# Kernel tuning notes

Measured on AMD Instinct MI355X. Metric: run time of the kernel, lower is better.

The kernel has to match this reference:

```python
import jax, jax.numpy as jnp
import numpy as np

N_HEAD = 8
WINDOW = 22   # sliding window size from get_mask()
TRAIN = 29    # per-segment length cap from get_mask()


def _build_mask(T):
    # Banded (sliding-window causal) mask on one segment, tiled 3x3 over segments.
    t = T // 3
    m = np.triu(np.ones((TRAIN, TRAIN), dtype=bool), 1)
    for i in range(WINDOW, TRAIN):
        m[i, : i - WINDOW + 1] = True
    m = np.tile(m[:t, :t], (3, 3))  # [T, T], True = masked out
    return jnp.asarray(m)


def setup_inputs() -> dict:
    key = jax.random.key(0)
    ks = jax.random.split(key, 5)
    B, T, C = 512, 87, 512
    s = 0.02
    return {
        "x": jax.random.normal(ks[0], (B, T, C), dtype=jnp.float32),
        "Wq": jax.random.normal(ks[1], (C, C), dtype=jnp.float32) * s,
        "bq": jnp.zeros((C,), dtype=jnp.float32),
        "Wk": jax.random.normal(ks[2], (C, C), dtype=jnp.float32) * s,
        "bk": jnp.zeros((C,), dtype=jnp.float32),
        "Wv": jax.random.normal(ks[3], (C, C), dtype=jnp.float32) * s,
        "bv": jnp.zeros((C,), dtype=jnp.float32),
        "Wp": jax.random.normal(ks[4], (C, C), dtype=jnp.float32) * s,
        "bp": jnp.zeros((C,), dtype=jnp.float32),
    }


def reference(x, Wq, bq, Wk, bk, Wv, bv, Wp, bp):
    B, T, C = x.shape
    H = N_HEAD
    D = C // H
    # nn.Linear: y = x @ W.T + b
    def split_heads(y):
        return y.reshape(B, T, H, D).transpose(0, 2, 1, 3)  # [B,H,T,D]
    q = split_heads(x @ Wq.T + bq)
    k = split_heads(x @ Wk.T + bk)
    v = split_heads(x @ Wv.T + bv)
    att = jnp.einsum("bhqd,bhkd->bhqk", q, k) * (1.0 / jnp.sqrt(jnp.float32(D)))
    mask = _build_mask(T)  # [T,T] True = disallowed
    att = jnp.where(mask[None, None], -jnp.inf, att)
    att = jax.nn.softmax(att, axis=-1)
    # dropout layers are identity in eval mode
    y = jnp.einsum("bhqk,bhkd->bhqd", att, v)
    y = y.transpose(0, 2, 1, 3).reshape(B, T, C)
    return y @ Wp.T + bp
```

## Files before the change

kernel.cpp:

```cpp
#include <hip/hip_runtime.h>
#include <hip/hip_bf16.h>
#include <stdint.h>

#define B_   512
#define T_   87
#define C_   512
#define H_   8
#define D_   64
#define BT_  44544
#define BH_  4096

typedef __attribute__((ext_vector_type(4))) float f32x4;
typedef __attribute__((ext_vector_type(8))) __bf16 bf16x8;
typedef __attribute__((ext_vector_type(4))) unsigned short u16x4;

__device__ __forceinline__ int mod29(int x) {
  return x < 29 ? x : (x < 58 ? x - 29 : x - 58);
}


__global__ void convert_x_kernel(const float* __restrict__ x,
                                 __hip_bfloat16* __restrict__ xb, int n4) {
  int stride = gridDim.x * blockDim.x;
  for (int i = blockIdx.x * blockDim.x + threadIdx.x; i < n4; i += stride) {
    f32x4 v = ((const f32x4*)x)[i];
    u16x4 o;
    o.x = __builtin_bit_cast(unsigned short, __float2bfloat16(v.x));
    o.y = __builtin_bit_cast(unsigned short, __float2bfloat16(v.y));
    o.z = __builtin_bit_cast(unsigned short, __float2bfloat16(v.z));
    o.w = __builtin_bit_cast(unsigned short, __float2bfloat16(v.w));
    ((u16x4*)xb)[i] = o;
  }
}

__global__ void convert_w_kernel(const float* __restrict__ Wq, const float* __restrict__ Wk,
                                 const float* __restrict__ Wv, const float* __restrict__ Wp,
                                 const float* __restrict__ bq, const float* __restrict__ bk,
                                 const float* __restrict__ bv,
                                 __hip_bfloat16* __restrict__ wqkv,
                                 __hip_bfloat16* __restrict__ wp,
                                 float* __restrict__ biasc) {
  const int NW = 262144;
  const int total = 3 * NW + NW + 1536;
  int stride = gridDim.x * blockDim.x;
  for (int i = blockIdx.x * blockDim.x + threadIdx.x; i < total; i += stride) {
    if (i < 3 * NW) {
      float v = (i < NW) ? Wq[i] : (i < 2 * NW ? Wk[i - NW] : Wv[i - 2 * NW]);
      wqkv[i] = __float2bfloat16(v);
    } else if (i < 4 * NW) {
      wp[i - 3 * NW] = __float2bfloat16(Wp[i - 3 * NW]);
    } else {
      int j = i - 4 * NW;
      biasc[j] = (j < 512) ? bq[j] : (j < 1024 ? bk[j - 512] : bv[j - 1024]);
    }
  }
}


template<int FM, int FN>
__device__ __forceinline__ void compute_tile(const char* Ab, const char* Bb,
                                             int wbM, int wbN, int r16, int r4,
                                             f32x4 acc[FM][FN]) {
  const int cxor = (r16 & 7) << 4;
  bf16x8 bf[FN][2];
#pragma unroll
  for (int fn = 0; fn < FN; ++fn) {
    int row = wbN + fn * 16 + r16;
#pragma unroll
    for (int kk = 0; kk < 2; ++kk)
      bf[fn][kk] = *(const bf16x8*)(Bb + row * 128 + ((kk * 64 + r4 * 16) ^ cxor));
  }
#pragma unroll
  for (int fm = 0; fm < FM; ++fm) {
    int row = wbM + fm * 16 + r16;
    bf16x8 a0 = *(const bf16x8*)(Ab + row * 128 + ((r4 * 16) ^ cxor));
    bf16x8 a1 = *(const bf16x8*)(Ab + row * 128 + ((64 + r4 * 16) ^ cxor));
#pragma unroll
    for (int fn = 0; fn < FN; ++fn) {
      acc[fm][fn] = __builtin_amdgcn_mfma_f32_16x16x32_bf16(a0, bf[fn][0], acc[fm][fn], 0, 0, 0);
      acc[fm][fn] = __builtin_amdgcn_mfma_f32_16x16x32_bf16(a1, bf[fn][1], acc[fm][fn], 0, 0, 0);
    }
  }
}

template<int EPI>
__global__ __launch_bounds__(256) void gemmr_kernel(
    const __hip_bfloat16* __restrict__ A, const __hip_bfloat16* __restrict__ Bt,
    const float* __restrict__ bias, int ntn,
    void* __restrict__ o0, void* __restrict__ o1, void* __restrict__ o2) {
  __shared__ __align__(16) char smem[2][2][16384];

  int tid = threadIdx.x, lane = tid & 63, wave = tid >> 6;
  int r16 = lane & 15, r4 = lane >> 4;

  int nwg = gridDim.x;
  int wg = (blockIdx.x & 7) * (nwg >> 3) + (blockIdx.x >> 3);
  int tileM = (wg / ntn) * 128, tileN = (wg % ntn) * 128;

  int wr = wave >> 1, wc = wave & 1;
  int wbM = wr * 64, wbN = wc * 64;

  const int rbase = tid >> 3, c = tid & 7;
  const int cs = (c ^ (rbase & 7)) << 4;
  const char* Ag = (const char*)A + (size_t)(tileM + rbase) * 1024 + c * 16;
  const char* Bg = (const char*)Bt + (size_t)(tileN + rbase) * 1024 + c * 16;

  f32x4 acc[4][4] = {};
  bf16x8 rA[4], rB[4];

#pragma unroll
  for (int j = 0; j < 4; ++j) {
    rA[j] = *(const bf16x8*)(Ag + (size_t)j * 32768);
    rB[j] = *(const bf16x8*)(Bg + (size_t)j * 32768);
  }
#pragma unroll
  for (int j = 0; j < 4; ++j) {
    *(bf16x8*)(&smem[0][0][0] + (rbase + 32 * j) * 128 + cs) = rA[j];
    *(bf16x8*)(&smem[0][1][0] + (rbase + 32 * j) * 128 + cs) = rB[j];
  }
  __syncthreads();

#pragma unroll
  for (int kt = 0; kt < 8; ++kt) {
    int cur = kt & 1;
    if (kt < 7) {
#pragma unroll
      for (int j = 0; j < 4; ++j) {
        rA[j] = *(const bf16x8*)(Ag + (size_t)j * 32768 + (kt + 1) * 128);
        rB[j] = *(const bf16x8*)(Bg + (size_t)j * 32768 + (kt + 1) * 128);
      }
    }
    __builtin_amdgcn_s_setprio(1);
    compute_tile<4, 4>(&smem[cur][0][0], &smem[cur][1][0], wbM, wbN, r16, r4, acc);
    __builtin_amdgcn_s_setprio(0);
    if (kt < 7) {
#pragma unroll
      for (int j = 0; j < 4; ++j) {
        *(bf16x8*)(&smem[cur ^ 1][0][0] + (rbase + 32 * j) * 128 + cs) = rA[j];
        *(bf16x8*)(&smem[cur ^ 1][1][0] + (rbase + 32 * j) * 128 + cs) = rB[j];
      }
    }
    __syncthreads();
  }

  if constexpr (EPI == 0) {
    char* scratch = &smem[0][0][0] + wave * 2304;
    int gn0 = tileN + wbN;
    int sel = gn0 >> 9;
    int hh = (gn0 & 511) >> 6;
    __hip_bfloat16* obase = (sel == 0) ? (__hip_bfloat16*)o0
                          : (sel == 1) ? (__hip_bfloat16*)o1 : (__hip_bfloat16*)o2;
#pragma unroll
    for (int fm = 0; fm < 4; ++fm) {
#pragma unroll
      for (int fn = 0; fn < 4; ++fn) {
        float bv = bias[gn0 + fn * 16 + r16];
#pragma unroll
        for (int rr = 0; rr < 4; ++rr)
          *(__hip_bfloat16*)(scratch + (r4 * 4 + rr) * 144 + (fn * 16 + r16) * 2) =
              __float2bfloat16(acc[fm][fn][rr] + bv);
      }
#pragma unroll
      for (int p = 0; p < 2; ++p) {
        bf16x8 vrow = *(const bf16x8*)(scratch + (p * 8 + (lane >> 3)) * 144 + (lane & 7) * 16);
        int gm = tileM + wbM + fm * 16 + p * 8 + (lane >> 3);
        int bb = gm / 87, tt = gm - bb * 87;
        *(bf16x8*)(obase + ((size_t)(bb * 8 + hh) * 96 + tt) * 64 + (lane & 7) * 8) = vrow;
      }
    }
  } else {
    char* scratch = &smem[0][0][0] + wave * 4352;
#pragma unroll
    for (int fm = 0; fm < 4; ++fm) {
#pragma unroll
      for (int fn = 0; fn < 4; ++fn) {
        float bv = bias[tileN + wbN + fn * 16 + r16];
#pragma unroll
        for (int rr = 0; rr < 4; ++rr)
          *(float*)(scratch + (r4 * 4 + rr) * 272 + (fn * 16 + r16) * 4) =
              acc[fm][fn][rr] + bv;
      }
#pragma unroll
      for (int p = 0; p < 4; ++p) {
        f32x4 vr = *(const f32x4*)(scratch + (p * 4 + (lane >> 4)) * 272 + (lane & 15) * 16);
        int gm = tileM + wbM + fm * 16 + p * 4 + (lane >> 4);
        *(f32x4*)((float*)o0 + (size_t)gm * 512 + tileN + wbN + (lane & 15) * 4) = vr;
      }
    }
  }
}

#define QS_O  0
#define KS_O  13824
#define VT_O  27648
#define PB_O  40960

__global__ __launch_bounds__(256) void attn_kernel(
    const __hip_bfloat16* __restrict__ q_ws, const __hip_bfloat16* __restrict__ k_ws,
    const __hip_bfloat16* __restrict__ v_ws, __hip_bfloat16* __restrict__ y_ws) {
  __shared__ __align__(16) char smem[60928];

  int tid = threadIdx.x, lane = tid & 63, wave = tid >> 6;
  int bh = blockIdx.x, b = bh >> 3, h = bh & 7;
  int r16 = lane & 15, r4 = lane >> 4;

  {
    const bf16x8* gq = (const bf16x8*)(q_ws + (size_t)bh * 6144);
    const bf16x8* gk = (const bf16x8*)(k_ws + (size_t)bh * 6144);
    const bf16x8* gv = (const bf16x8*)(v_ws + (size_t)bh * 6144);
    for (int i = tid; i < 768; i += 256) {
      int row = i >> 3, ch = i & 7;
      *(bf16x8*)(smem + QS_O + row * 144 + ch * 16) = gq[i];
      *(bf16x8*)(smem + KS_O + row * 144 + ch * 16) = gk[i];
      bf16x8 v8 = gv[i];
      int tc = row >> 3, tb = (row & 7) << 1, xr = ch & 3;
#pragma unroll
      for (int e = 0; e < 8; ++e) {
        int d = ch * 8 + e;
        *(__bf16*)(smem + VT_O + d * 208 + ((tc ^ xr) << 4) + tb) = v8[e];
      }
    }
  }
  __syncthreads();

  int ljv[6]; bool cok[6];
#pragma unroll
  for (int j = 0; j < 6; ++j) {
    int col = j * 16 + r16;
    ljv[j] = mod29(col);
    cok[j] = col < 87;
  }

  for (int m = wave; m < 6; m += 4) {
    f32x4 s[6] = {};
#pragma unroll
    for (int kk = 0; kk < 2; ++kk) {
      bf16x8 aq = *(const bf16x8*)(smem + QS_O + (m * 16 + r16) * 144 + kk * 64 + r4 * 16);
#pragma unroll
      for (int j = 0; j < 6; ++j) {
        bf16x8 kb = *(const bf16x8*)(smem + KS_O + (j * 16 + r16) * 144 + kk * 64 + r4 * 16);
        s[j] = __builtin_amdgcn_mfma_f32_16x16x32_bf16(aq, kb, s[j], 0, 0, 0);
      }
    }
#pragma unroll
    for (int rr = 0; rr < 4; ++rr) {
      int row = m * 16 + r4 * 4 + rr;
      bool rok = row < 87;
      int lr = mod29(row);
      float mxv = -1e30f;
#pragma unroll
      for (int j = 0; j < 6; ++j) {
        bool al = rok && cok[j] && (ljv[j] <= lr) && (ljv[j] + 21 >= lr);
        float sv = al ? s[j][rr] * 0.125f : -1e30f;
        s[j][rr] = sv;
        mxv = fmaxf(mxv, sv);
      }
      mxv = fmaxf(mxv, __shfl_xor(mxv, 1));
      mxv = fmaxf(mxv, __shfl_xor(mxv, 2));
      mxv = fmaxf(mxv, __shfl_xor(mxv, 4));
      mxv = fmaxf(mxv, __shfl_xor(mxv, 8));
      float sm = 0.f;
#pragma unroll
      for (int j = 0; j < 6; ++j) {
        float e = __expf(s[j][rr] - mxv);
        s[j][rr] = e;
        sm += e;
      }
      sm += __shfl_xor(sm, 1);
      sm += __shfl_xor(sm, 2);
      sm += __shfl_xor(sm, 4);
      sm += __shfl_xor(sm, 8);
      float inv = rok ? 1.f / sm : 0.f;
#pragma unroll
      for (int j = 0; j < 6; ++j)
        *(__hip_bfloat16*)(smem + PB_O + row * 208 + (j * 16 + r16) * 2) =
            __float2bfloat16(s[j][rr] * inv);
    }
  }
  __syncthreads();

  for (int p = 0; p < 6; ++p) {
    int pair = wave + p * 4;
    int mt = pair >> 2, nt = pair & 3;
    int d = nt * 16 + r16;
    int dx = (d >> 3) & 3;
    f32x4 acc = {0.f, 0.f, 0.f, 0.f};
#pragma unroll
    for (int kk = 0; kk < 3; ++kk) {
      bf16x8 a  = *(const bf16x8*)(smem + PB_O + (mt * 16 + r16) * 208 + kk * 64 + r4 * 16);
      bf16x8 bb = *(const bf16x8*)(smem + VT_O + d * 208 + (((kk * 4 + r4) ^ dx) << 4));
      acc = __builtin_amdgcn_mfma_f32_16x16x32_bf16(a, bb, acc, 0, 0, 0);
    }
    int t0 = mt * 16 + r4 * 4;
#pragma unroll
    for (int r = 0; r < 4; ++r) {
      int t = t0 + r;
      if (t < 87)
        y_ws[((size_t)b * 87 + t) * 512 + h * 64 + d] = __float2bfloat16(acc[r]);
    }
  }
}

extern "C" void kernel_launch(void* const* d_in, const int* in_sizes, int n_in,
                              void* d_out, int out_size, void* d_ws, size_t ws_size,
                              hipStream_t stream) {
  const float* x  = (const float*)d_in[0];
  const float* Wq = (const float*)d_in[1];
  const float* bq = (const float*)d_in[2];
  const float* Wk = (const float*)d_in[3];
  const float* bk = (const float*)d_in[4];
  const float* Wv = (const float*)d_in[5];
  const float* bv = (const float*)d_in[6];
  const float* Wp = (const float*)d_in[7];
  const float* bp = (const float*)d_in[8];
  float* out = (float*)d_out;

  char* ws = (char*)d_ws;
  size_t off = 0;
  __hip_bfloat16* xb    = (__hip_bfloat16*)(ws + off); off += (size_t)BT_ * 512 * 2;
  __hip_bfloat16* wqkv  = (__hip_bfloat16*)(ws + off); off += 1536 * 512 * 2;
  __hip_bfloat16* wp    = (__hip_bfloat16*)(ws + off); off += 512 * 512 * 2;
  float*          biasc = (float*)(ws + off);          off += 8192;
  __hip_bfloat16* q_ws  = (__hip_bfloat16*)(ws + off); off += (size_t)BH_ * 6144 * 2;
  __hip_bfloat16* k_ws  = (__hip_bfloat16*)(ws + off); off += (size_t)BH_ * 6144 * 2;
  __hip_bfloat16* v_ws  = (__hip_bfloat16*)(ws + off); off += (size_t)BH_ * 6144 * 2;
  __hip_bfloat16* yb = xb;

  if (ws_size < off) return;

  convert_x_kernel<<<2048, 256, 0, stream>>>(x, xb, BT_ * 512 / 4);
  convert_w_kernel<<<1024, 256, 0, stream>>>(Wq, Wk, Wv, Wp, bq, bk, bv, wqkv, wp, biasc);
  gemmr_kernel<0><<<4176, 256, 0, stream>>>(xb, wqkv, biasc, 12, q_ws, k_ws, v_ws);
  attn_kernel<<<BH_, 256, 0, stream>>>(q_ws, k_ws, v_ws, yb);
  gemmr_kernel<1><<<1392, 256, 0, stream>>>(yb, wp, bp, 4, out, nullptr, nullptr);
}
```

Measured before the change: 237.7 us.

## Fuse x fp32-to-bf16 conversion into QKV GEMM and coalesce attention output stores

Removes the separate convert_x kernel. The QKV GEMM now reads fp32 x directly and converts it to bf16 while staging into shared memory, which saves a full write and re-read of the bf16 copy of x. The catch is that each of the 12 N-tiles re-reads the fp32 A rows, so A-side global traffic per tile doubles. Separately, the attention kernel now stages its output through LDS and writes 16-byte rows, replacing scattered 2-byte stores.

```diff
diff --git a/kernel.cpp b/kernel.cpp
--- a/kernel.cpp
+++ b/kernel.cpp
@@ -13,24 +13,23 @@
 typedef __attribute__((ext_vector_type(4))) float f32x4;
 typedef __attribute__((ext_vector_type(8))) __bf16 bf16x8;
 typedef __attribute__((ext_vector_type(4))) unsigned short u16x4;
+typedef __attribute__((ext_vector_type(8))) unsigned short u16x8;
 
 __device__ __forceinline__ int mod29(int x) {
   return x < 29 ? x : (x < 58 ? x - 29 : x - 58);
 }
 
-
-__global__ void convert_x_kernel(const float* __restrict__ x,
-                                 __hip_bfloat16* __restrict__ xb, int n4) {
-  int stride = gridDim.x * blockDim.x;
-  for (int i = blockIdx.x * blockDim.x + threadIdx.x; i < n4; i += stride) {
-    f32x4 v = ((const f32x4*)x)[i];
-    u16x4 o;
-    o.x = __builtin_bit_cast(unsigned short, __float2bfloat16(v.x));
-    o.y = __builtin_bit_cast(unsigned short, __float2bfloat16(v.y));
-    o.z = __builtin_bit_cast(unsigned short, __float2bfloat16(v.z));
-    o.w = __builtin_bit_cast(unsigned short, __float2bfloat16(v.w));
-    ((u16x4*)xb)[i] = o;
-  }
+__device__ __forceinline__ bf16x8 cvt8(f32x4 a, f32x4 b) {
+  u16x8 u;
+  u[0] = __builtin_bit_cast(unsigned short, __float2bfloat16(a.x));
+  u[1] = __builtin_bit_cast(unsigned short, __float2bfloat16(a.y));
+  u[2] = __builtin_bit_cast(unsigned short, __float2bfloat16(a.z));
+  u[3] = __builtin_bit_cast(unsigned short, __float2bfloat16(a.w));
+  u[4] = __builtin_bit_cast(unsigned short, __float2bfloat16(b.x));
+  u[5] = __builtin_bit_cast(unsigned short, __float2bfloat16(b.y));
+  u[6] = __builtin_bit_cast(unsigned short, __float2bfloat16(b.z));
+  u[7] = __builtin_bit_cast(unsigned short, __float2bfloat16(b.w));
+  return __builtin_bit_cast(bf16x8, u);
 }
 
 __global__ void convert_w_kernel(const float* __restrict__ Wq, const float* __restrict__ Wk,
@@ -56,7 +55,6 @@
   }
 }
 
-
 template<int FM, int FN>
 __device__ __forceinline__ void compute_tile(const char* Ab, const char* Bb,
                                              int wbM, int wbN, int r16, int r4,
@@ -83,10 +81,9 @@
   }
 }
 
-template<int EPI>
-__global__ __launch_bounds__(256) void gemmr_kernel(
-    const __hip_bfloat16* __restrict__ A, const __hip_bfloat16* __restrict__ Bt,
-    const float* __restrict__ bias, int ntn,
+__global__ __launch_bounds__(256) void gemmq_kernel(
+    const float* __restrict__ A, const __hip_bfloat16* __restrict__ Bt,
+    const float* __restrict__ bias,
     void* __restrict__ o0, void* __restrict__ o1, void* __restrict__ o2) {
   __shared__ __align__(16) char smem[2][2][16384];
 
@@ -95,27 +92,29 @@
 
   int nwg = gridDim.x;
   int wg = (blockIdx.x & 7) * (nwg >> 3) + (blockIdx.x >> 3);
-  int tileM = (wg / ntn) * 128, tileN = (wg % ntn) * 128;
+  int tileM = (wg / 12) * 128, tileN = (wg % 12) * 128;
 
   int wr = wave >> 1, wc = wave & 1;
   int wbM = wr * 64, wbN = wc * 64;
 
   const int rbase = tid >> 3, c = tid & 7;
   const int cs = (c ^ (rbase & 7)) << 4;
-  const char* Ag = (const char*)A + (size_t)(tileM + rbase) * 1024 + c * 16;
+  const char* Ag = (const char*)A + (size_t)(tileM + rbase) * 2048 + c * 32;
   const char* Bg = (const char*)Bt + (size_t)(tileN + rbase) * 1024 + c * 16;
 
   f32x4 acc[4][4] = {};
-  bf16x8 rA[4], rB[4];
+  f32x4 rAf[8];
+  bf16x8 rB[4];
 
 #pragma unroll
   for (int j = 0; j < 4; ++j) {
-    rA[j] = *(const bf16x8*)(Ag + (size_t)j * 32768);
+    rAf[2 * j]     = *(const f32x4*)(Ag + (size_t)j * 65536);
+    rAf[2 * j + 1] = *(const f32x4*)(Ag + (size_t)j * 65536 + 16);
     rB[j] = *(const bf16x8*)(Bg + (size_t)j * 32768);
   }
 #pragma unroll
   for (int j = 0; j < 4; ++j) {
-    *(bf16x8*)(&smem[0][0][0] + (rbase + 32 * j) * 128 + cs) = rA[j];
+    *(bf16x8*)(&smem[0][0][0] + (rbase + 32 * j) * 128 + cs) = cvt8(rAf[2 * j], rAf[2 * j + 1]);
     *(bf16x8*)(&smem[0][1][0] + (rbase + 32 * j) * 128 + cs) = rB[j];
   }
   __syncthreads();
@@ -126,7 +125,8 @@
     if (kt < 7) {
 #pragma unroll
       for (int j = 0; j < 4; ++j) {
-        rA[j] = *(const bf16x8*)(Ag + (size_t)j * 32768 + (kt + 1) * 128);
+        rAf[2 * j]     = *(const f32x4*)(Ag + (size_t)j * 65536 + (kt + 1) * 256);
+        rAf[2 * j + 1] = *(const f32x4*)(Ag + (size_t)j * 65536 + (kt + 1) * 256 + 16);
         rB[j] = *(const bf16x8*)(Bg + (size_t)j * 32768 + (kt + 1) * 128);
       }
     }
@@ -136,14 +136,14 @@
     if (kt < 7) {
 #pragma unroll
       for (int j = 0; j < 4; ++j) {
-        *(bf16x8*)(&smem[cur ^ 1][0][0] + (rbase + 32 * j) * 128 + cs) = rA[j];
+        *(bf16x8*)(&smem[cur ^ 1][0][0] + (rbase + 32 * j) * 128 + cs) = cvt8(rAf[2 * j], rAf[2 * j + 1]);
         *(bf16x8*)(&smem[cur ^ 1][1][0] + (rbase + 32 * j) * 128 + cs) = rB[j];
       }
     }
     __syncthreads();
   }
 
-  if constexpr (EPI == 0) {
+  {
     char* scratch = &smem[0][0][0] + wave * 2304;
     int gn0 = tileN + wbN;
     int sel = gn0 >> 9;
@@ -168,7 +168,68 @@
         *(bf16x8*)(obase + ((size_t)(bb * 8 + hh) * 96 + tt) * 64 + (lane & 7) * 8) = vrow;
       }
     }
-  } else {
+  }
+}
+
+__global__ __launch_bounds__(256) void gemmr_kernel(
+    const __hip_bfloat16* __restrict__ A, const __hip_bfloat16* __restrict__ Bt,
+    const float* __restrict__ bias, int ntn, float* __restrict__ out) {
+  __shared__ __align__(16) char smem[2][2][16384];
+
+  int tid = threadIdx.x, lane = tid & 63, wave = tid >> 6;
+  int r16 = lane & 15, r4 = lane >> 4;
+
+  int nwg = gridDim.x;
+  int wg = (blockIdx.x & 7) * (nwg >> 3) + (blockIdx.x >> 3);
+  int tileM = (wg / ntn) * 128, tileN = (wg % ntn) * 128;
+
+  int wr = wave >> 1, wc = wave & 1;
+  int wbM = wr * 64, wbN = wc * 64;
+
+  const int rbase = tid >> 3, c = tid & 7;
+  const int cs = (c ^ (rbase & 7)) << 4;
+  const char* Ag = (const char*)A + (size_t)(tileM + rbase) * 1024 + c * 16;
+  const char* Bg = (const char*)Bt + (size_t)(tileN + rbase) * 1024 + c * 16;
+
+  f32x4 acc[4][4] = {};
+  bf16x8 rA[4], rB[4];
+
+#pragma unroll
+  for (int j = 0; j < 4; ++j) {
+    rA[j] = *(const bf16x8*)(Ag + (size_t)j * 32768);
+    rB[j] = *(const bf16x8*)(Bg + (size_t)j * 32768);
+  }
+#pragma unroll
+  for (int j = 0; j < 4; ++j) {
+    *(bf16x8*)(&smem[0][0][0] + (rbase + 32 * j) * 128 + cs) = rA[j];
+    *(bf16x8*)(&smem[0][1][0] + (rbase + 32 * j) * 128 + cs) = rB[j];
+  }
+  __syncthreads();
+
+#pragma unroll
+  for (int kt = 0; kt < 8; ++kt) {
+    int cur = kt & 1;
+    if (kt < 7) {
+#pragma unroll
+      for (int j = 0; j < 4; ++j) {
+        rA[j] = *(const bf16x8*)(Ag + (size_t)j * 32768 + (kt + 1) * 128);
+        rB[j] = *(const bf16x8*)(Bg + (size_t)j * 32768 + (kt + 1) * 128);
+      }
+    }
+    __builtin_amdgcn_s_setprio(1);
+    compute_tile<4, 4>(&smem[cur][0][0], &smem[cur][1][0], wbM, wbN, r16, r4, acc);
+    __builtin_amdgcn_s_setprio(0);
+    if (kt < 7) {
+#pragma unroll
+      for (int j = 0; j < 4; ++j) {
+        *(bf16x8*)(&smem[cur ^ 1][0][0] + (rbase + 32 * j) * 128 + cs) = rA[j];
+        *(bf16x8*)(&smem[cur ^ 1][1][0] + (rbase + 32 * j) * 128 + cs) = rB[j];
+      }
+    }
+    __syncthreads();
+  }
+
+  {
     char* scratch = &smem[0][0][0] + wave * 4352;
 #pragma unroll
     for (int fm = 0; fm < 4; ++fm) {
@@ -184,7 +245,7 @@
       for (int p = 0; p < 4; ++p) {
         f32x4 vr = *(const f32x4*)(scratch + (p * 4 + (lane >> 4)) * 272 + (lane & 15) * 16);
         int gm = tileM + wbM + fm * 16 + p * 4 + (lane >> 4);
-        *(f32x4*)((float*)o0 + (size_t)gm * 512 + tileN + wbN + (lane & 15) * 4) = vr;
+        *(f32x4*)(out + (size_t)gm * 512 + tileN + wbN + (lane & 15) * 4) = vr;
       }
     }
   }
@@ -293,10 +354,17 @@
     }
     int t0 = mt * 16 + r4 * 4;
 #pragma unroll
-    for (int r = 0; r < 4; ++r) {
-      int t = t0 + r;
-      if (t < 87)
-        y_ws[((size_t)b * 87 + t) * 512 + h * 64 + d] = __float2bfloat16(acc[r]);
+    for (int r = 0; r < 4; ++r)
+      *(__bf16*)(smem + QS_O + (t0 + r) * 136 + d * 2) =
+          __builtin_bit_cast(__bf16, (unsigned short)__builtin_bit_cast(unsigned short, __float2bfloat16(acc[r])));
+  }
+  __syncthreads();
+
+  for (int i = tid; i < 768; i += 256) {
+    int row = i >> 3, ch = i & 7;
+    if (row < 87) {
+      bf16x8 vrow = *(const bf16x8*)(smem + QS_O + row * 136 + ch * 16);
+      *(bf16x8*)((char*)y_ws + ((size_t)b * 87 + row) * 1024 + h * 128 + ch * 16) = vrow;
     }
   }
 }
@@ -317,20 +385,18 @@
 
   char* ws = (char*)d_ws;
   size_t off = 0;
-  __hip_bfloat16* xb    = (__hip_bfloat16*)(ws + off); off += (size_t)BT_ * 512 * 2;
+  __hip_bfloat16* yb    = (__hip_bfloat16*)(ws + off); off += (size_t)BT_ * 512 * 2;
   __hip_bfloat16* wqkv  = (__hip_bfloat16*)(ws + off); off += 1536 * 512 * 2;
   __hip_bfloat16* wp    = (__hip_bfloat16*)(ws + off); off += 512 * 512 * 2;
   float*          biasc = (float*)(ws + off);          off += 8192;
   __hip_bfloat16* q_ws  = (__hip_bfloat16*)(ws + off); off += (size_t)BH_ * 6144 * 2;
   __hip_bfloat16* k_ws  = (__hip_bfloat16*)(ws + off); off += (size_t)BH_ * 6144 * 2;
   __hip_bfloat16* v_ws  = (__hip_bfloat16*)(ws + off); off += (size_t)BH_ * 6144 * 2;
-  __hip_bfloat16* yb = xb;
 
   if (ws_size < off) return;
 
-  convert_x_kernel<<<2048, 256, 0, stream>>>(x, xb, BT_ * 512 / 4);
   convert_w_kernel<<<1024, 256, 0, stream>>>(Wq, Wk, Wv, Wp, bq, bk, bv, wqkv, wp, biasc);
-  gemmr_kernel<0><<<4176, 256, 0, stream>>>(xb, wqkv, biasc, 12, q_ws, k_ws, v_ws);
+  gemmq_kernel<<<4176, 256, 0, stream>>>(x, wqkv, biasc, q_ws, k_ws, v_ws);
   attn_kernel<<<BH_, 256, 0, stream>>>(q_ws, k_ws, v_ws, yb);
-  gemmr_kernel<1><<<1392, 256, 0, stream>>>(yb, wp, bp, 4, out, nullptr, nullptr);
-}
+  gemmr_kernel<<<1392, 256, 0, stream>>>(yb, wp, bp, 4, out);
+}
```

New measurement: 269.2 us. +13.3%, slower.

## Rewrite GEMMs as 256x256 8-wave tiles with direct global-to-LDS 4-stage pipeline

Applied to the files above, without the earlier changes.

Replaces the 128x128 4-wave GEMM with a 256x256, 512-thread kernel that stages A/B panels straight into LDS using global_load_lds, ring-buffered over four slots with explicit vmcnt waits and barriers that interleave loads with MFMA phases. The goal is more reuse per LDS byte, no register round-trip for staging, and overlap of memory with compute. The XCD-aware block remap now handles grids that are not a multiple of 8. Separately, the attention epilogue stages its output through LDS so it can write coalesced 16-byte rows instead of scattered scalar bf16 stores. The trade-offs are fewer workgroups (1044 and 348), which may lower occupancy and hurt tail balance, and heavier LDS use.

```diff
diff --git a/kernel.cpp b/kernel.cpp
--- a/kernel.cpp
+++ b/kernel.cpp
@@ -13,6 +13,17 @@
 typedef __attribute__((ext_vector_type(4))) float f32x4;
 typedef __attribute__((ext_vector_type(8))) __bf16 bf16x8;
 typedef __attribute__((ext_vector_type(4))) unsigned short u16x4;
+
+__device__ __forceinline__ void gl_lds16(const void* g, void* l) {
+  __builtin_amdgcn_global_load_lds(
+      (const __attribute__((address_space(1))) unsigned int*)g,
+      (__attribute__((address_space(3))) unsigned int*)l, 16, 0, 0);
+}
+
+template<int N>
+__device__ __forceinline__ void waitv() {
+  asm volatile("s_waitcnt vmcnt(%0)" :: "i"(N) : "memory");
+}
 
 __device__ __forceinline__ int mod29(int x) {
   return x < 29 ? x : (x < 58 ? x - 29 : x - 58);
@@ -57,101 +68,126 @@
 }
 
 
-template<int FM, int FN>
-__device__ __forceinline__ void compute_tile(const char* Ab, const char* Bb,
-                                             int wbM, int wbN, int r16, int r4,
-                                             f32x4 acc[FM][FN]) {
-  const int cxor = (r16 & 7) << 4;
-  bf16x8 bf[FN][2];
-#pragma unroll
-  for (int fn = 0; fn < FN; ++fn) {
-    int row = wbN + fn * 16 + r16;
-#pragma unroll
-    for (int kk = 0; kk < 2; ++kk)
-      bf[fn][kk] = *(const bf16x8*)(Bb + row * 128 + ((kk * 64 + r4 * 16) ^ cxor));
-  }
-#pragma unroll
-  for (int fm = 0; fm < FM; ++fm) {
-    int row = wbM + fm * 16 + r16;
-    bf16x8 a0 = *(const bf16x8*)(Ab + row * 128 + ((r4 * 16) ^ cxor));
-    bf16x8 a1 = *(const bf16x8*)(Ab + row * 128 + ((64 + r4 * 16) ^ cxor));
-#pragma unroll
-    for (int fn = 0; fn < FN; ++fn) {
-      acc[fm][fn] = __builtin_amdgcn_mfma_f32_16x16x32_bf16(a0, bf[fn][0], acc[fm][fn], 0, 0, 0);
-      acc[fm][fn] = __builtin_amdgcn_mfma_f32_16x16x32_bf16(a1, bf[fn][1], acc[fm][fn], 0, 0, 0);
-    }
-  }
-}
+__device__ __forceinline__ void stage_panel(const char* g, int kbyte, char* dst,
+                                            int wave, int lane) {
+  int rl = lane >> 2, s = lane & 3;
+#pragma unroll
+  for (int j = 0; j < 2; ++j) {
+    int rbase = j * 128 + wave * 16;
+    int row = rbase + rl;
+    int colsw = ((s ^ ((row >> 1) & 3)) << 4);
+    gl_lds16(g + (size_t)row * 1024 + kbyte + colsw, dst + rbase * 64);
+  }
+}
+
+#define PHASE_SEP() __builtin_amdgcn_sched_barrier(0)
 
 template<int EPI>
-__global__ __launch_bounds__(256) void gemmr_kernel(
+__global__ __launch_bounds__(512, 2) void gemm8_kernel(
     const __hip_bfloat16* __restrict__ A, const __hip_bfloat16* __restrict__ Bt,
     const float* __restrict__ bias, int ntn,
     void* __restrict__ o0, void* __restrict__ o1, void* __restrict__ o2) {
-  __shared__ __align__(16) char smem[2][2][16384];
+  constexpr int SLOT = 32768;
+  constexpr int BOFF = 16384;
+  __shared__ __align__(16) char smem[4 * SLOT];
 
   int tid = threadIdx.x, lane = tid & 63, wave = tid >> 6;
   int r16 = lane & 15, r4 = lane >> 4;
 
   int nwg = gridDim.x;
-  int wg = (blockIdx.x & 7) * (nwg >> 3) + (blockIdx.x >> 3);
-  int tileM = (wg / ntn) * 128, tileN = (wg % ntn) * 128;
-
-  int wr = wave >> 1, wc = wave & 1;
-  int wbM = wr * 64, wbN = wc * 64;
-
-  const int rbase = tid >> 3, c = tid & 7;
-  const int cs = (c ^ (rbase & 7)) << 4;
-  const char* Ag = (const char*)A + (size_t)(tileM + rbase) * 1024 + c * 16;
-  const char* Bg = (const char*)Bt + (size_t)(tileN + rbase) * 1024 + c * 16;
-
-  f32x4 acc[4][4] = {};
-  bf16x8 rA[4], rB[4];
-
-#pragma unroll
-  for (int j = 0; j < 4; ++j) {
-    rA[j] = *(const bf16x8*)(Ag + (size_t)j * 32768);
-    rB[j] = *(const bf16x8*)(Bg + (size_t)j * 32768);
-  }
-#pragma unroll
-  for (int j = 0; j < 4; ++j) {
-    *(bf16x8*)(&smem[0][0][0] + (rbase + 32 * j) * 128 + cs) = rA[j];
-    *(bf16x8*)(&smem[0][1][0] + (rbase + 32 * j) * 128 + cs) = rB[j];
-  }
-  __syncthreads();
-
-#pragma unroll
-  for (int kt = 0; kt < 8; ++kt) {
-    int cur = kt & 1;
-    if (kt < 7) {
-#pragma unroll
-      for (int j = 0; j < 4; ++j) {
-        rA[j] = *(const bf16x8*)(Ag + (size_t)j * 32768 + (kt + 1) * 128);
-        rB[j] = *(const bf16x8*)(Bg + (size_t)j * 32768 + (kt + 1) * 128);
-      }
-    }
+  int xcd = blockIdx.x & 7, idx = blockIdx.x >> 3;
+  int q8 = nwg >> 3, r8 = nwg & 7;
+  int wg = (xcd < r8 ? xcd * (q8 + 1) : r8 * (q8 + 1) + (xcd - r8) * q8) + idx;
+  int tileM = (wg / ntn) * 256, tileN = (wg % ntn) * 256;
+
+  int wr = wave >> 2, wc = wave & 3;
+  int wbM = wr * 128, wbN = wc * 64;
+
+  f32x4 acc[8][4] = {};
+
+  const char* Ag = (const char*)A + (size_t)tileM * 1024;
+  const char* Bg = (const char*)Bt + (size_t)tileN * 1024;
+
+  int arow[8], brow[4];
+#pragma unroll
+  for (int fm = 0; fm < 8; ++fm) arow[fm] = wbM + fm * 16 + r16;
+#pragma unroll
+  for (int fn = 0; fn < 4; ++fn) brow[fn] = wbN + fn * 16 + r16;
+
+  stage_panel(Ag, 0, smem, wave, lane);
+  stage_panel(Bg, 0, smem + BOFF, wave, lane);
+  stage_panel(Ag, 64, smem + SLOT, wave, lane);
+  stage_panel(Bg, 64, smem + SLOT + BOFF, wave, lane);
+
+#pragma unroll
+  for (int kt = 0; kt < 16; ++kt) {
+    if (kt < 15) waitv<4>(); else waitv<0>();
+    PHASE_SEP();
+    __builtin_amdgcn_s_barrier();
+    PHASE_SEP();
+
+    const char* cb = smem + (kt & 3) * SLOT;
+    char* nb = smem + ((kt + 2) & 3) * SLOT;
+    bool st = kt < 14;
+
+    bf16x8 bfr[4], afr[4];
+#pragma unroll
+    for (int fn = 0; fn < 4; ++fn)
+      bfr[fn] = *(const bf16x8*)(cb + BOFF + brow[fn] * 64 +
+                                 ((r4 ^ ((brow[fn] >> 1) & 3)) << 4));
+#pragma unroll
+    for (int fm = 0; fm < 4; ++fm)
+      afr[fm] = *(const bf16x8*)(cb + arow[fm] * 64 +
+                                 ((r4 ^ ((arow[fm] >> 1) & 3)) << 4));
+    if (st) stage_panel(Ag, (kt + 2) * 64, nb, wave, lane);
+    PHASE_SEP();
+    __builtin_amdgcn_s_barrier();
+    asm volatile("s_waitcnt lgkmcnt(0)" ::: "memory");
+    PHASE_SEP();
     __builtin_amdgcn_s_setprio(1);
-    compute_tile<4, 4>(&smem[cur][0][0], &smem[cur][1][0], wbM, wbN, r16, r4, acc);
+#pragma unroll
+    for (int fm = 0; fm < 4; ++fm)
+#pragma unroll
+      for (int fn = 0; fn < 4; ++fn)
+        acc[fm][fn] = __builtin_amdgcn_mfma_f32_16x16x32_bf16(afr[fm], bfr[fn],
+                                                              acc[fm][fn], 0, 0, 0);
     __builtin_amdgcn_s_setprio(0);
-    if (kt < 7) {
-#pragma unroll
-      for (int j = 0; j < 4; ++j) {
-        *(bf16x8*)(&smem[cur ^ 1][0][0] + (rbase + 32 * j) * 128 + cs) = rA[j];
-        *(bf16x8*)(&smem[cur ^ 1][1][0] + (rbase + 32 * j) * 128 + cs) = rB[j];
-      }
-    }
-    __syncthreads();
+    PHASE_SEP();
+    __builtin_amdgcn_s_barrier();
+    PHASE_SEP();
+
+    bf16x8 afr2[4];
+#pragma unroll
+    for (int fm = 0; fm < 4; ++fm)
+      afr2[fm] = *(const bf16x8*)(cb + arow[fm + 4] * 64 +
+                                  ((r4 ^ ((arow[fm + 4] >> 1) & 3)) << 4));
+    if (st) stage_panel(Bg, (kt + 2) * 64, nb + BOFF, wave, lane);
+    PHASE_SEP();
+    __builtin_amdgcn_s_barrier();
+    asm volatile("s_waitcnt lgkmcnt(0)" ::: "memory");
+    PHASE_SEP();
+    __builtin_amdgcn_s_setprio(1);
+#pragma unroll
+    for (int fm = 0; fm < 4; ++fm)
+#pragma unroll
+      for (int fn = 0; fn < 4; ++fn)
+        acc[fm + 4][fn] = __builtin_amdgcn_mfma_f32_16x16x32_bf16(afr2[fm], bfr[fn],
+                                                                  acc[fm + 4][fn], 0, 0, 0);
+    __builtin_amdgcn_s_setprio(0);
+    PHASE_SEP();
+    __builtin_amdgcn_s_barrier();
+    PHASE_SEP();
   }
 
   if constexpr (EPI == 0) {
-    char* scratch = &smem[0][0][0] + wave * 2304;
+    char* scratch = smem + wave * 2304;
     int gn0 = tileN + wbN;
     int sel = gn0 >> 9;
     int hh = (gn0 & 511) >> 6;
     __hip_bfloat16* obase = (sel == 0) ? (__hip_bfloat16*)o0
                           : (sel == 1) ? (__hip_bfloat16*)o1 : (__hip_bfloat16*)o2;
 #pragma unroll
-    for (int fm = 0; fm < 4; ++fm) {
+    for (int fm = 0; fm < 8; ++fm) {
 #pragma unroll
       for (int fn = 0; fn < 4; ++fn) {
         float bv = bias[gn0 + fn * 16 + r16];
@@ -169,9 +205,9 @@
       }
     }
   } else {
-    char* scratch = &smem[0][0][0] + wave * 4352;
-#pragma unroll
-    for (int fm = 0; fm < 4; ++fm) {
+    char* scratch = smem + wave * 4352;
+#pragma unroll
+    for (int fm = 0; fm < 8; ++fm) {
 #pragma unroll
       for (int fn = 0; fn < 4; ++fn) {
         float bv = bias[tileN + wbN + fn * 16 + r16];
@@ -293,10 +329,17 @@
     }
     int t0 = mt * 16 + r4 * 4;
 #pragma unroll
-    for (int r = 0; r < 4; ++r) {
-      int t = t0 + r;
-      if (t < 87)
-        y_ws[((size_t)b * 87 + t) * 512 + h * 64 + d] = __float2bfloat16(acc[r]);
+    for (int r = 0; r < 4; ++r)
+      *(__bf16*)(smem + QS_O + (t0 + r) * 136 + d * 2) =
+          __builtin_bit_cast(__bf16, __builtin_bit_cast(unsigned short, __float2bfloat16(acc[r])));
+  }
+  __syncthreads();
+
+  for (int i = tid; i < 768; i += 256) {
+    int row = i >> 3, ch = i & 7;
+    if (row < 87) {
+      bf16x8 vrow = *(const bf16x8*)(smem + QS_O + row * 136 + ch * 16);
+      *(bf16x8*)((char*)y_ws + ((size_t)b * 87 + row) * 1024 + h * 128 + ch * 16) = vrow;
     }
   }
 }
@@ -330,7 +373,7 @@
 
   convert_x_kernel<<<2048, 256, 0, stream>>>(x, xb, BT_ * 512 / 4);
   convert_w_kernel<<<1024, 256, 0, stream>>>(Wq, Wk, Wv, Wp, bq, bk, bv, wqkv, wp, biasc);
-  gemmr_kernel<0><<<4176, 256, 0, stream>>>(xb, wqkv, biasc, 12, q_ws, k_ws, v_ws);
+  gemm8_kernel<0><<<1044, 512, 0, stream>>>(xb, wqkv, biasc, 6, q_ws, k_ws, v_ws);
   attn_kernel<<<BH_, 256, 0, stream>>>(q_ws, k_ws, v_ws, yb);
-  gemmr_kernel<1><<<1392, 256, 0, stream>>>(yb, wp, bp, 4, out, nullptr, nullptr);
-}
+  gemm8_kernel<1><<<348, 512, 0, stream>>>(yb, wp, bp, 2, out, nullptr, nullptr);
+}
```

Result: slower. 249.0 us (+4.7%).

## Fuse QKV projection with per-head attention in one kernel

Applied to the files above, without the earlier changes.

Replaces the separate QKV GEMM and attention kernels with a single kernel per (batch, head). It computes that head's Q, K and V tile from x directly into shared memory, then runs masked softmax attention and writes y. This removes the global round-trip of the Q/K/V workspaces and one launch. In exchange, each workgroup reads its batch's x rows and streams its head's weight slice straight from global memory without LDS staging, so x is re-read 8 times (once per head). The 64 KB LDS footprint and wide accumulator array may also lower occupancy.

```diff
diff --git a/kernel.cpp b/kernel.cpp
--- a/kernel.cpp
+++ b/kernel.cpp
@@ -56,6 +56,208 @@
   }
 }
 
+#define FX_O  0
+#define FQS_O 24576
+#define FKS_O 38400
+#define FVT_O 52224
+#define FPB_O 0
+#define FYS_O 24576
+
+__global__ __launch_bounds__(256) void fused_qa_kernel(
+    const __hip_bfloat16* __restrict__ xb, const __hip_bfloat16* __restrict__ wqkv,
+    const float* __restrict__ biasc, __hip_bfloat16* __restrict__ y_ws) {
+  __shared__ __align__(16) char smem[65536];
+
+  int tid = threadIdx.x, lane = tid & 63, wave = tid >> 6;
+  int r16 = lane & 15, r4 = lane >> 4;
+
+  int wg = (blockIdx.x & 7) * 512 + (blockIdx.x >> 3);
+  int b = wg >> 3, h = wg & 7;
+
+  const char* xg = (const char*)xb + (size_t)b * 87 * 1024;
+
+  const char* wrow[3];
+#pragma unroll
+  for (int f = 0; f < 3; ++f) {
+    int gf = wave * 3 + f;
+    int sel = gf >> 2;
+    int row = sel * 512 + h * 64 + (gf & 3) * 16 + r16;
+    wrow[f] = (const char*)wqkv + (size_t)row * 1024;
+  }
+
+  const int rbase = tid >> 3, c = tid & 7;
+
+  f32x4 acc[6][3] = {};
+
+  {
+#pragma unroll
+    for (int j = 0; j < 3; ++j) {
+      int row = rbase + 32 * j;
+      bf16x8 v = {};
+      if (row < 87) v = *(const bf16x8*)(xg + (size_t)row * 1024 + c * 16);
+      *(bf16x8*)(smem + FX_O + row * 128 + ((c ^ (row & 7)) << 4)) = v;
+    }
+  }
+  __syncthreads();
+
+#pragma unroll
+  for (int kt = 0; kt < 8; ++kt) {
+    const int cur = kt & 1;
+    bf16x8 rx[3];
+    if (kt < 7) {
+#pragma unroll
+      for (int j = 0; j < 3; ++j) {
+        int row = rbase + 32 * j;
+        bf16x8 v = {};
+        if (row < 87) v = *(const bf16x8*)(xg + (size_t)row * 1024 + (kt + 1) * 128 + c * 16);
+        rx[j] = v;
+      }
+    }
+    bf16x8 bw[3][2];
+#pragma unroll
+    for (int f = 0; f < 3; ++f)
+#pragma unroll
+      for (int kk = 0; kk < 2; ++kk)
+        bw[f][kk] = *(const bf16x8*)(wrow[f] + kt * 128 + kk * 64 + r4 * 16);
+    const char* xls = smem + FX_O + cur * 12288;
+    __builtin_amdgcn_s_setprio(1);
+#pragma unroll
+    for (int fm = 0; fm < 6; ++fm) {
+      int arow = fm * 16 + r16;
+      int cx = (arow & 7) << 4;
+      bf16x8 a0 = *(const bf16x8*)(xls + arow * 128 + ((r4 * 16) ^ cx));
+      bf16x8 a1 = *(const bf16x8*)(xls + arow * 128 + ((64 + r4 * 16) ^ cx));
+#pragma unroll
+      for (int fn = 0; fn < 3; ++fn) {
+        acc[fm][fn] = __builtin_amdgcn_mfma_f32_16x16x32_bf16(a0, bw[fn][0], acc[fm][fn], 0, 0, 0);
+        acc[fm][fn] = __builtin_amdgcn_mfma_f32_16x16x32_bf16(a1, bw[fn][1], acc[fm][fn], 0, 0, 0);
+      }
+    }
+    __builtin_amdgcn_s_setprio(0);
+    if (kt < 7) {
+#pragma unroll
+      for (int j = 0; j < 3; ++j) {
+        int row = rbase + 32 * j;
+        *(bf16x8*)(smem + FX_O + (cur ^ 1) * 12288 + row * 128 + ((c ^ (row & 7)) << 4)) = rx[j];
+      }
+    }
+    __syncthreads();
+  }
+
+#pragma unroll
+  for (int fn = 0; fn < 3; ++fn) {
+    int gf = wave * 3 + fn;
+    int sel = gf >> 2;
+    float bv = biasc[sel * 512 + h * 64 + (gf & 3) * 16 + r16];
+    if (sel < 2) {
+      int base = (sel == 0) ? FQS_O : FKS_O;
+      int cl = (gf & 3) * 16 + r16;
+#pragma unroll
+      for (int fm = 0; fm < 6; ++fm)
+#pragma unroll
+        for (int rr = 0; rr < 4; ++rr) {
+          int row = fm * 16 + r4 * 4 + rr;
+          *(__hip_bfloat16*)(smem + base + row * 144 + cl * 2) =
+              __float2bfloat16(acc[fm][fn][rr] + bv);
+        }
+    } else {
+      int d = (gf & 3) * 16 + r16;
+      int dx = (d >> 3) & 3;
+#pragma unroll
+      for (int fm = 0; fm < 6; ++fm)
+#pragma unroll
+        for (int rr = 0; rr < 4; ++rr) {
+          int t = fm * 16 + r4 * 4 + rr;
+          *(__hip_bfloat16*)(smem + FVT_O + d * 208 + (((t >> 3) ^ dx) << 4) + (t & 7) * 2) =
+              __float2bfloat16(acc[fm][fn][rr] + bv);
+        }
+    }
+  }
+  __syncthreads();
+
+  int ljv[6]; bool cok[6];
+#pragma unroll
+  for (int j = 0; j < 6; ++j) {
+    int col = j * 16 + r16;
+    ljv[j] = mod29(col);
+    cok[j] = col < 87;
+  }
+
+  for (int m = wave; m < 6; m += 4) {
+    f32x4 s[6] = {};
+#pragma unroll
+    for (int kk = 0; kk < 2; ++kk) {
+      bf16x8 aq = *(const bf16x8*)(smem + FQS_O + (m * 16 + r16) * 144 + kk * 64 + r4 * 16);
+#pragma unroll
+      for (int j = 0; j < 6; ++j) {
+        bf16x8 kb = *(const bf16x8*)(smem + FKS_O + (j * 16 + r16) * 144 + kk * 64 + r4 * 16);
+        s[j] = __builtin_amdgcn_mfma_f32_16x16x32_bf16(aq, kb, s[j], 0, 0, 0);
+      }
+    }
+#pragma unroll
+    for (int rr = 0; rr < 4; ++rr) {
+      int row = m * 16 + r4 * 4 + rr;
+      bool rok = row < 87;
+      int lr = mod29(row);
+      float mxv = -1e30f;
+#pragma unroll
+      for (int j = 0; j < 6; ++j) {
+        bool al = rok && cok[j] && (ljv[j] <= lr) && (ljv[j] + 21 >= lr);
+        float sv = al ? s[j][rr] * 0.125f : -1e30f;
+        s[j][rr] = sv;
+        mxv = fmaxf(mxv, sv);
+      }
+      mxv = fmaxf(mxv, __shfl_xor(mxv, 1));
+      mxv = fmaxf(mxv, __shfl_xor(mxv, 2));
+      mxv = fmaxf(mxv, __shfl_xor(mxv, 4));
+      mxv = fmaxf(mxv, __shfl_xor(mxv, 8));
+      float sm = 0.f;
+#pragma unroll
+      for (int j = 0; j < 6; ++j) {
+        float e = __expf(s[j][rr] - mxv);
+        s[j][rr] = e;
+        sm += e;
+      }
+      sm += __shfl_xor(sm, 1);
+      sm += __shfl_xor(sm, 2);
+      sm += __shfl_xor(sm, 4);
+      sm += __shfl_xor(sm, 8);
+      float inv = rok ? 1.f / sm : 0.f;
+#pragma unroll
+      for (int j = 0; j < 6; ++j)
+        *(__hip_bfloat16*)(smem + FPB_O + row * 208 + (j * 16 + r16) * 2) =
+            __float2bfloat16(s[j][rr] * inv);
+    }
+  }
+  __syncthreads();
+
+  for (int p = 0; p < 6; ++p) {
+    int pair = wave + p * 4;
+    int mt = pair >> 2, nt = pair & 3;
+    int d = nt * 16 + r16;
+    int dx = (d >> 3) & 3;
+    f32x4 a2 = {0.f, 0.f, 0.f, 0.f};
+#pragma unroll
+    for (int kk = 0; kk < 3; ++kk) {
+      bf16x8 a  = *(const bf16x8*)(smem + FPB_O + (mt * 16 + r16) * 208 + kk * 64 + r4 * 16);
+      bf16x8 bb = *(const bf16x8*)(smem + FVT_O + d * 208 + (((kk * 4 + r4) ^ dx) << 4));
+      a2 = __builtin_amdgcn_mfma_f32_16x16x32_bf16(a, bb, a2, 0, 0, 0);
+    }
+    int t0 = mt * 16 + r4 * 4;
+#pragma unroll
+    for (int r = 0; r < 4; ++r)
+      *(__hip_bfloat16*)(smem + FYS_O + (t0 + r) * 136 + d * 2) = __float2bfloat16(a2[r]);
+  }
+  __syncthreads();
+
+  for (int i = tid; i < 768; i += 256) {
+    int row = i >> 3, ch = i & 7;
+    if (row < 87) {
+      bf16x8 vrow = *(const bf16x8*)(smem + FYS_O + row * 136 + ch * 16);
+      *(bf16x8*)((char*)y_ws + ((size_t)b * 87 + row) * 1024 + h * 128 + ch * 16) = vrow;
+    }
+  }
+}
 
 template<int FM, int FN>
 __device__ __forceinline__ void compute_tile(const char* Ab, const char* Bb,
@@ -83,11 +285,9 @@
   }
 }
 
-template<int EPI>
 __global__ __launch_bounds__(256) void gemmr_kernel(
     const __hip_bfloat16* __restrict__ A, const __hip_bfloat16* __restrict__ Bt,
-    const float* __restrict__ bias, int ntn,
-    void* __restrict__ o0, void* __restrict__ o1, void* __restrict__ o2) {
+    const float* __restrict__ bias, int ntn, float* __restrict__ out) {
   __shared__ __align__(16) char smem[2][2][16384];
 
   int tid = threadIdx.x, lane = tid & 63, wave = tid >> 6;
@@ -143,32 +343,7 @@
     __syncthreads();
   }
 
-  if constexpr (EPI == 0) {
-    char* scratch = &smem[0][0][0] + wave * 2304;
-    int gn0 = tileN + wbN;
-    int sel = gn0 >> 9;
-    int hh = (gn0 & 511) >> 6;
-    __hip_bfloat16* obase = (sel == 0) ? (__hip_bfloat16*)o0
-                          : (sel == 1) ? (__hip_bfloat16*)o1 : (__hip_bfloat16*)o2;
-#pragma unroll
-    for (int fm = 0; fm < 4; ++fm) {
-#pragma unroll
-      for (int fn = 0; fn < 4; ++fn) {
-        float bv = bias[gn0 + fn * 16 + r16];
-#pragma unroll
-        for (int rr = 0; rr < 4; ++rr)
-          *(__hip_bfloat16*)(scratch + (r4 * 4 + rr) * 144 + (fn * 16 + r16) * 2) =
-              __float2bfloat16(acc[fm][fn][rr] + bv);
-      }
-#pragma unroll
-      for (int p = 0; p < 2; ++p) {
-        bf16x8 vrow = *(const bf16x8*)(scratch + (p * 8 + (lane >> 3)) * 144 + (lane & 7) * 16);
-        int gm = tileM + wbM + fm * 16 + p * 8 + (lane >> 3);
-        int bb = gm / 87, tt = gm - bb * 87;
-        *(bf16x8*)(obase + ((size_t)(bb * 8 + hh) * 96 + tt) * 64 + (lane & 7) * 8) = vrow;
-      }
-    }
-  } else {
+  {
     char* scratch = &smem[0][0][0] + wave * 4352;
 #pragma unroll
     for (int fm = 0; fm < 4; ++fm) {
@@ -184,119 +359,8 @@
       for (int p = 0; p < 4; ++p) {
         f32x4 vr = *(const f32x4*)(scratch + (p * 4 + (lane >> 4)) * 272 + (lane & 15) * 16);
         int gm = tileM + wbM + fm * 16 + p * 4 + (lane >> 4);
-        *(f32x4*)((float*)o0 + (size_t)gm * 512 + tileN + wbN + (lane & 15) * 4) = vr;
-      }
-    }
-  }
-}
-
-#define QS_O  0
-#define KS_O  13824
-#define VT_O  27648
-#define PB_O  40960
-
-__global__ __launch_bounds__(256) void attn_kernel(
-    const __hip_bfloat16* __restrict__ q_ws, const __hip_bfloat16* __restrict__ k_ws,
-    const __hip_bfloat16* __restrict__ v_ws, __hip_bfloat16* __restrict__ y_ws) {
-  __shared__ __align__(16) char smem[60928];
-
-  int tid = threadIdx.x, lane = tid & 63, wave = tid >> 6;
-  int bh = blockIdx.x, b = bh >> 3, h = bh & 7;
-  int r16 = lane & 15, r4 = lane >> 4;
-
-  {
-    const bf16x8* gq = (const bf16x8*)(q_ws + (size_t)bh * 6144);
-    const bf16x8* gk = (const bf16x8*)(k_ws + (size_t)bh * 6144);
-    const bf16x8* gv = (const bf16x8*)(v_ws + (size_t)bh * 6144);
-    for (int i = tid; i < 768; i += 256) {
-      int row = i >> 3, ch = i & 7;
-      *(bf16x8*)(smem + QS_O + row * 144 + ch * 16) = gq[i];
-      *(bf16x8*)(smem + KS_O + row * 144 + ch * 16) = gk[i];
-      bf16x8 v8 = gv[i];
-      int tc = row >> 3, tb = (row & 7) << 1, xr = ch & 3;
-#pragma unroll
-      for (int e = 0; e < 8; ++e) {
-        int d = ch * 8 + e;
-        *(__bf16*)(smem + VT_O + d * 208 + ((tc ^ xr) << 4) + tb) = v8[e];
-      }
-    }
-  }
-  __syncthreads();
-
-  int ljv[6]; bool cok[6];
-#pragma unroll
-  for (int j = 0; j < 6; ++j) {
-    int col = j * 16 + r16;
-    ljv[j] = mod29(col);
-    cok[j] = col < 87;
-  }
-
-  for (int m = wave; m < 6; m += 4) {
-    f32x4 s[6] = {};
-#pragma unroll
-    for (int kk = 0; kk < 2; ++kk) {
-      bf16x8 aq = *(const bf16x8*)(smem + QS_O + (m * 16 + r16) * 144 + kk * 64 + r4 * 16);
-#pragma unroll
-      for (int j = 0; j < 6; ++j) {
-        bf16x8 kb = *(const bf16x8*)(smem + KS_O + (j * 16 + r16) * 144 + kk * 64 + r4 * 16);
-        s[j] = __builtin_amdgcn_mfma_f32_16x16x32_bf16(aq, kb, s[j], 0, 0, 0);
-      }
-    }
-#pragma unroll
-    for (int rr = 0; rr < 4; ++rr) {
-      int row = m * 16 + r4 * 4 + rr;
-      bool rok = row < 87;
-      int lr = mod29(row);
-      float mxv = -1e30f;
-#pragma unroll
-      for (int j = 0; j < 6; ++j) {
-        bool al = rok && cok[j] && (ljv[j] <= lr) && (ljv[j] + 21 >= lr);
-        float sv = al ? s[j][rr] * 0.125f : -1e30f;
-        s[j][rr] = sv;
-        mxv = fmaxf(mxv, sv);
-      }
-      mxv = fmaxf(mxv, __shfl_xor(mxv, 1));
-      mxv = fmaxf(mxv, __shfl_xor(mxv, 2));
-      mxv = fmaxf(mxv, __shfl_xor(mxv, 4));
-      mxv = fmaxf(mxv, __shfl_xor(mxv, 8));
-      float sm = 0.f;
-#pragma unroll
-      for (int j = 0; j < 6; ++j) {
-        float e = __expf(s[j][rr] - mxv);
-        s[j][rr] = e;
-        sm += e;
-      }
-      sm += __shfl_xor(sm, 1);
-      sm += __shfl_xor(sm, 2);
-      sm += __shfl_xor(sm, 4);
-      sm += __shfl_xor(sm, 8);
-      float inv = rok ? 1.f / sm : 0.f;
-#pragma unroll
-      for (int j = 0; j < 6; ++j)
-        *(__hip_bfloat16*)(smem + PB_O + row * 208 + (j * 16 + r16) * 2) =
-            __float2bfloat16(s[j][rr] * inv);
-    }
-  }
-  __syncthreads();
-
-  for (int p = 0; p < 6; ++p) {
-    int pair = wave + p * 4;
-    int mt = pair >> 2, nt = pair & 3;
-    int d = nt * 16 + r16;
-    int dx = (d >> 3) & 3;
-    f32x4 acc = {0.f, 0.f, 0.f, 0.f};
-#pragma unroll
-    for (int kk = 0; kk < 3; ++kk) {
-      bf16x8 a  = *(const bf16x8*)(smem + PB_O + (mt * 16 + r16) * 208 + kk * 64 + r4 * 16);
-      bf16x8 bb = *(const bf16x8*)(smem + VT_O + d * 208 + (((kk * 4 + r4) ^ dx) << 4));
-      acc = __builtin_amdgcn_mfma_f32_16x16x32_bf16(a, bb, acc, 0, 0, 0);
-    }
-    int t0 = mt * 16 + r4 * 4;
-#pragma unroll
-    for (int r = 0; r < 4; ++r) {
-      int t = t0 + r;
-      if (t < 87)
-        y_ws[((size_t)b * 87 + t) * 512 + h * 64 + d] = __float2bfloat16(acc[r]);
+        *(f32x4*)(out + (size_t)gm * 512 + tileN + wbN + (lane & 15) * 4) = vr;
+      }
     }
   }
 }
@@ -318,19 +382,15 @@
   char* ws = (char*)d_ws;
   size_t off = 0;
   __hip_bfloat16* xb    = (__hip_bfloat16*)(ws + off); off += (size_t)BT_ * 512 * 2;
+  __hip_bfloat16* yb    = (__hip_bfloat16*)(ws + off); off += (size_t)BT_ * 512 * 2;
   __hip_bfloat16* wqkv  = (__hip_bfloat16*)(ws + off); off += 1536 * 512 * 2;
   __hip_bfloat16* wp    = (__hip_bfloat16*)(ws + off); off += 512 * 512 * 2;
   float*          biasc = (float*)(ws + off);          off += 8192;
-  __hip_bfloat16* q_ws  = (__hip_bfloat16*)(ws + off); off += (size_t)BH_ * 6144 * 2;
-  __hip_bfloat16* k_ws  = (__hip_bfloat16*)(ws + off); off += (size_t)BH_ * 6144 * 2;
-  __hip_bfloat16* v_ws  = (__hip_bfloat16*)(ws + off); off += (size_t)BH_ * 6144 * 2;
-  __hip_bfloat16* yb = xb;
 
   if (ws_size < off) return;
 
   convert_x_kernel<<<2048, 256, 0, stream>>>(x, xb, BT_ * 512 / 4);
   convert_w_kernel<<<1024, 256, 0, stream>>>(Wq, Wk, Wv, Wp, bq, bk, bv, wqkv, wp, biasc);
-  gemmr_kernel<0><<<4176, 256, 0, stream>>>(xb, wqkv, biasc, 12, q_ws, k_ws, v_ws);
-  attn_kernel<<<BH_, 256, 0, stream>>>(q_ws, k_ws, v_ws, yb);
-  gemmr_kernel<1><<<1392, 256, 0, stream>>>(yb, wp, bp, 4, out, nullptr, nullptr);
-}
+  fused_qa_kernel<<<BH_, 256, 0, stream>>>(xb, wqkv, biasc, yb);
+  gemmr_kernel<<<1392, 256, 0, stream>>>(yb, wp, bp, 4, out);
+}
```

New measurement: 249.6 us. 1.05x slower.
